# Optimization experiments

Measured on AMD Instinct MI355X. Metric: run time of the kernel, lower is better.

Reference implementation:

```python
import jax, jax.numpy as jnp
import numpy as np
from jax import lax

B, T, D_MODEL = 4, 2048, 2048
EXPAND, D_CONV = 2, 4
D_INNER = D_MODEL * EXPAND


def setup_inputs() -> dict:
    key = jax.random.key(0)
    ks = jax.random.split(key, 5)
    x = jax.random.normal(ks[0], (B, T, D_MODEL), dtype=jnp.float32)
    w_in = jax.random.normal(ks[1], (2 * D_INNER, D_MODEL), dtype=jnp.float32) * (D_MODEL ** -0.5)
    w_out = jax.random.normal(ks[2], (D_MODEL, D_INNER), dtype=jnp.float32) * (D_INNER ** -0.5)
    conv_w = jax.random.normal(ks[3], (D_INNER, 1, D_CONV), dtype=jnp.float32) * (D_CONV ** -0.5)
    conv_b = jax.random.normal(ks[4], (D_INNER,), dtype=jnp.float32) * 0.02
    D = jnp.ones((D_INNER,), dtype=jnp.float32)
    return {"x": x, "w_in": w_in, "w_out": w_out, "conv_w": conv_w, "conv_b": conv_b, "D": D}


def _forward(x, w_in, w_out, conv_w, conv_b, D):
    # in_proj: [B,T,C] @ [C, 2*d_inner]
    x_proj = jnp.einsum('btc,dc->btd', x, w_in)
    xi, gate = jnp.split(x_proj, 2, axis=-1)  # each [B,T,d_inner]
    # depthwise causal conv1d: torch pads both sides by d_conv-1 then truncates
    # output to first T positions -> equivalent to left-pad (d_conv-1), valid conv.
    xc = jnp.transpose(xi, (0, 2, 1))  # [B, d_inner, T]
    xc = lax.conv_general_dilated(
        xc, conv_w,
        window_strides=(1,),
        padding=[(D_CONV - 1, 0)],
        dimension_numbers=('NCH', 'OIH', 'NCH'),
        feature_group_count=D_INNER,
    ) + conv_b[None, :, None]
    xc = jnp.transpose(xc, (0, 2, 1))  # [B, T, d_inner]
    h = jax.nn.silu(xc) * D[None, None, :] * jax.nn.silu(gate)
    return jnp.einsum('btd,cd->btc', h, w_out)


def reference(x, w_in, w_out, conv_w, conv_b, D):
    return _forward(x, w_in, w_out, conv_w, conv_b, D)
```

## Files before the change

### kernel.cpp

```cpp
#include <hip/hip_runtime.h>
#include <hip/hip_bf16.h>
#include <stdint.h>
#include <string.h>


#define BT_TOTAL 8192
#define DM 2048
#define DI 4096

typedef __attribute__((ext_vector_type(8)))  short short8;
typedef __attribute__((ext_vector_type(16))) float f32x16;

__device__ __forceinline__ void async_ld16(const void* g, void* l) {
    __builtin_amdgcn_global_load_lds(
        (__attribute__((address_space(1))) void*)g,
        (__attribute__((address_space(3))) void*)l,
        16, 0, 0);
}

__device__ __forceinline__ float bf2f(ushort u) {
    union { uint i; float f; } v; v.i = ((uint)u) << 16; return v.f;
}

__device__ __forceinline__ ushort f2bf_bits(float f) {
    union { __hip_bfloat16 b; ushort u; } v;
    v.b = __float2bfloat16(f);
    return v.u;
}

#define RA0 0
#define RB0 16384
#define RA1 32768
#define RB1 49152

#define BAR()   asm volatile("s_barrier" ::: "memory")
#define VM6()   asm volatile("s_waitcnt vmcnt(6)" ::: "memory")
#define VM0()   asm volatile("s_waitcnt vmcnt(0)" ::: "memory")
#define PRIO1() __builtin_amdgcn_s_setprio(1)
#define PRIO0() __builtin_amdgcn_s_setprio(0)

template<bool OUT_BF16>
__global__ __launch_bounds__(512, 2) void gemm256_kernel(
    const ushort* __restrict__ A, const ushort* __restrict__ B,
    void* __restrict__ Cp, int M, int N, int K)
{
    __shared__ ushort lds[65536];

    const int tid  = threadIdx.x;
    const int lane = tid & 63;
    const int wave = tid >> 6;
    const int wm   = wave >> 2;
    const int wn   = wave & 3;
    const int l31  = lane & 31;
    const int half = lane >> 5;

    const int nbx = gridDim.x;
    const int nwg = nbx * gridDim.y;
    const int orig = blockIdx.y * nbx + blockIdx.x;
    const int xcd  = orig & 7;
    const int t    = orig >> 3;
    const int sloc = t >> 5;
    const int u    = t & 31;
    const int spx  = (nwg >> 5) >> 3;
    const int g    = xcd * spx + sloc;
    const int scols = nbx >> 2;
    const int sr   = g / scols;
    const int sc   = g - sr * scols;
    const int bm   = (sr * 8 + (u >> 2)) * 256;
    const int bn   = (sc * 4 + (u & 3)) * 256;

    const int rq = tid >> 3;
    const int jq = tid & 7;
    const int fq = (rq ^ (rq >> 3)) & 7;
    const int goffA = (bm + rq) * K + ((jq ^ fq) * 8);
    const int goffB = (bn + rq) * K + ((jq ^ fq) * 8);
    const int dst8  = tid * 8;

    const int flane = (l31 ^ (l31 >> 3)) & 7;
    const int cl8   = (half ^ flane) * 8;
    const int aBase = (wm * 128 + l31) * 64;
    const int bBase = (wn * 64  + l31) * 64;

    f32x16 acc[4][2];
#pragma unroll
    for (int m = 0; m < 4; ++m)
#pragma unroll
        for (int n = 0; n < 2; ++n)
#pragma unroll
            for (int r = 0; r < 16; ++r)
                acc[m][n][r] = 0.f;

    short8 aE[4], aO[4], b0[4], b1[4];

#define STA(P, QROW, REG) async_ld16((P) + (size_t)(QROW) * K + goffA, \
                                     &lds[(REG) + (QROW) * 64 + dst8])
#define STB(P, QROW, REG) async_ld16((P) + (size_t)(QROW) * K + goffB, \
                                     &lds[(REG) + (QROW) * 64 + dst8])

#define RDA(MH, REG) do { \
    _Pragma("unroll") \
    for (int ks = 0; ks < 4; ++ks) { \
        aE[ks] = *(const short8*)&lds[(REG) + aBase + (MH)*4096 + (cl8 ^ (ks<<4))]; \
        aO[ks] = *(const short8*)&lds[(REG) + aBase + (MH)*4096 + 2048 + (cl8 ^ (ks<<4) ^ 32)]; \
    } } while (0)

#define RDB(DSTV, NF, REG) do { \
    _Pragma("unroll") \
    for (int ks = 0; ks < 4; ++ks) { \
        DSTV[ks] = *(const short8*)&lds[(REG) + bBase + (NF)*2048 + (cl8 ^ (ks<<4) ^ ((NF)<<5))]; \
    } } while (0)

#define MMA(MH, NH, BF) do { \
    _Pragma("unroll") \
    for (int ks = 0; ks < 4; ++ks) { \
        acc[(MH)*2    ][(NH)] = __builtin_amdgcn_mfma_f32_32x32x16_bf16( \
            aE[ks], BF[ks], acc[(MH)*2    ][(NH)], 0, 0, 0); \
        acc[(MH)*2 + 1][(NH)] = __builtin_amdgcn_mfma_f32_32x32x16_bf16( \
            aO[ks], BF[ks], acc[(MH)*2 + 1][(NH)], 0, 0, 0); \
    } } while (0)

    {
        STA(A, 0, RA0);  STA(A, 128, RA0);
        STB(B, 0, RB0);  STB(B, 128, RB0);
        STA(A, 64, RA0); STA(A, 192, RA0);
        STB(B, 64, RB0); STB(B, 192, RB0);
        const ushort* Ap = A + 64;
        const ushort* Bp = B + 64;
        STA(Ap, 0, RA1);  STA(Ap, 128, RA1);
        STB(Bp, 0, RB1);  STB(Bp, 128, RB1);
        STA(Ap, 64, RA1); STA(Ap, 192, RA1);
        VM6(); BAR();
    }

    const int NITER = K >> 7;
    for (int i = 0; i < NITER; ++i) {
        const bool last = (i == NITER - 1);
        const int k1 = 128 * i + 64;
        const int k2 = 128 * i + 128;
        const int k3 = 128 * i + 192;

        RDA(0, RA0); RDB(b0, 0, RB0);
        STB(B + k1, 64, RB1); STB(B + k1, 192, RB1);
        PRIO1(); MMA(0, 0, b0); PRIO0();
        BAR();

        RDB(b1, 1, RB0);
        if (!last) { STA(A + k2, 0, RA0); STA(A + k2, 128, RA0); }
        PRIO1(); MMA(0, 1, b1); PRIO0();
        BAR();

        RDA(1, RA0);
        if (!last) { STB(B + k2, 0, RB0); STB(B + k2, 128, RB0); }
        PRIO1(); MMA(1, 1, b1); PRIO0();
        BAR();

        if (!last) { STA(A + k2, 64, RA0); STA(A + k2, 192, RA0); }
        PRIO1(); MMA(1, 0, b0); PRIO0();
        if (last) { VM0(); } else { VM6(); }
        BAR();

        RDA(0, RA1); RDB(b0, 0, RB1);
        if (!last) { STB(B + k2, 64, RB0); STB(B + k2, 192, RB0); }
        PRIO1(); MMA(0, 0, b0); PRIO0();
        BAR();

        RDB(b1, 1, RB1);
        if (!last) { STA(A + k3, 0, RA1); STA(A + k3, 128, RA1); }
        PRIO1(); MMA(0, 1, b1); PRIO0();
        BAR();

        RDA(1, RA1);
        if (!last) { STB(B + k3, 0, RB1); STB(B + k3, 128, RB1); }
        PRIO1(); MMA(1, 1, b1); PRIO0();
        BAR();

        if (!last) { STA(A + k3, 64, RA1); STA(A + k3, 192, RA1); }
        PRIO1(); MMA(1, 0, b0); PRIO0();
        if (!last) { VM6(); BAR(); }
    }

    const int col0 = bn + wn * 64 + l31;
    const int row0 = bm + wm * 128 + 4 * half;
    if (OUT_BF16) {
        __hip_bfloat16* C = (__hip_bfloat16*)Cp;
#pragma unroll
        for (int m = 0; m < 4; ++m)
#pragma unroll
            for (int n = 0; n < 2; ++n)
#pragma unroll
                for (int r = 0; r < 16; ++r) {
                    const int row = row0 + m * 32 + (r & 3) + 8 * (r >> 2);
                    C[(size_t)row * (size_t)N + col0 + n * 32] =
                        __float2bfloat16(acc[m][n][r]);
                }
    } else {
        float* C = (float*)Cp;
#pragma unroll
        for (int m = 0; m < 4; ++m)
#pragma unroll
            for (int n = 0; n < 2; ++n)
#pragma unroll
                for (int r = 0; r < 16; ++r) {
                    const int row = row0 + m * 32 + (r & 3) + 8 * (r >> 2);
                    C[(size_t)row * (size_t)N + col0 + n * 32] = acc[m][n][r];
                }
    }
}

__global__ __launch_bounds__(256) void conv_silu_kernel(
    const ushort* __restrict__ xp,
    const float* __restrict__ cw,
    const float* __restrict__ cb,
    const float* __restrict__ Dv,
    ushort* __restrict__ h)
{
    const int v  = blockIdx.x * 256 + threadIdx.x;
    const int d8 = (v & 511) * 8;
    const int bt = v >> 9;
    const int t  = bt & 2047;

    const uint4 gv = *(const uint4*)(xp + (size_t)bt * (2 * DI) + DI + d8);
    uint4 tap[4];
#pragma unroll
    for (int k = 0; k < 4; ++k) {
        const int tt = t - 3 + k;
        if (tt >= 0)
            tap[k] = *(const uint4*)(xp + (size_t)(bt - 3 + k) * (2 * DI) + d8);
        else
            tap[k] = (uint4){0u, 0u, 0u, 0u};
    }

    const float4* cwv = (const float4*)(cw + (size_t)d8 * 4);
    const float4  cb0 = *(const float4*)(cb + d8);
    const float4  cb1 = *(const float4*)(cb + d8 + 4);
    const float4  dv0 = *(const float4*)(Dv + d8);
    const float4  dv1 = *(const float4*)(Dv + d8 + 4);
    const float cbs[8] = {cb0.x, cb0.y, cb0.z, cb0.w, cb1.x, cb1.y, cb1.z, cb1.w};
    const float dvs[8] = {dv0.x, dv0.y, dv0.z, dv0.w, dv1.x, dv1.y, dv1.z, dv1.w};

    ushort res[8];
#pragma unroll
    for (int j = 0; j < 8; ++j) {
        float a = cbs[j];
        const float4 w = cwv[j];
        const float wk[4] = {w.x, w.y, w.z, w.w};
#pragma unroll
        for (int k = 0; k < 4; ++k) {
            const uint u = ((const uint*)&tap[k])[j >> 1];
            const ushort us = (j & 1) ? (ushort)(u >> 16) : (ushort)(u & 0xffff);
            a += bf2f(us) * wk[k];
        }
        const uint gu = ((const uint*)&gv)[j >> 1];
        const ushort gs = (j & 1) ? (ushort)(gu >> 16) : (ushort)(gu & 0xffff);
        const float g = bf2f(gs);
        const float sc = a / (1.f + __expf(-a));
        const float sg = g / (1.f + __expf(-g));
        res[j] = f2bf_bits(sc * dvs[j] * sg);
    }
    *(uint4*)(h + (size_t)bt * DI + d8) = *(const uint4*)res;
}

__global__ __launch_bounds__(256) void f32_to_bf16_x4(
    const float* __restrict__ in, __hip_bfloat16* __restrict__ out, int n4)
{
    const int i = blockIdx.x * 256 + threadIdx.x;
    if (i >= n4) return;
    const float4 v = *(const float4*)(in + (size_t)i * 4);
    union { __hip_bfloat16 hh[4]; ushort4 u; } cv;
    cv.hh[0] = __float2bfloat16(v.x);
    cv.hh[1] = __float2bfloat16(v.y);
    cv.hh[2] = __float2bfloat16(v.z);
    cv.hh[3] = __float2bfloat16(v.w);
    *(ushort4*)((ushort*)out + (size_t)i * 4) = cv.u;
}

extern "C" void kernel_launch(void* const* d_in, const int* in_sizes, int n_in,
                              void* d_out, int out_size, void* d_ws, size_t ws_size,
                              hipStream_t stream)
{
    const float* x     = (const float*)d_in[0];
    const float* w_in  = (const float*)d_in[1];
    const float* w_out = (const float*)d_in[2];
    const float* cw    = (const float*)d_in[3];
    const float* cb    = (const float*)d_in[4];
    const float* Dv    = (const float*)d_in[5];
    float* out = (float*)d_out;

    char* wsc = (char*)d_ws;
    __hip_bfloat16* xproj = (__hip_bfloat16*)wsc;
    __hip_bfloat16* xb    = (__hip_bfloat16*)(wsc + (size_t)134217728);
    __hip_bfloat16* winb  = (__hip_bfloat16*)(wsc + (size_t)134217728 + 33554432);
    __hip_bfloat16* hbuf  = (__hip_bfloat16*)(wsc + (size_t)134217728);
    __hip_bfloat16* woutb = (__hip_bfloat16*)(wsc + (size_t)201326592);

    f32_to_bf16_x4<<<(BT_TOTAL * DM / 4 + 255) / 256, 256, 0, stream>>>(x, xb, BT_TOTAL * DM / 4);
    f32_to_bf16_x4<<<(2 * DI * DM / 4 + 255) / 256, 256, 0, stream>>>(w_in, winb, 2 * DI * DM / 4);
    f32_to_bf16_x4<<<(DM * DI / 4 + 255) / 256, 256, 0, stream>>>(w_out, woutb, DM * DI / 4);

    gemm256_kernel<true><<<dim3((2 * DI) / 256, BT_TOTAL / 256), 512, 0, stream>>>(
        (const ushort*)xb, (const ushort*)winb, xproj, BT_TOTAL, 2 * DI, DM);

    conv_silu_kernel<<<(BT_TOTAL * DI / 8) / 256, 256, 0, stream>>>(
        (const ushort*)xproj, cw, cb, Dv, (ushort*)hbuf);

    gemm256_kernel<false><<<dim3(DM / 256, BT_TOTAL / 256), 512, 0, stream>>>(
        (const ushort*)hbuf, (const ushort*)woutb, out, BT_TOTAL, DM, DI);
}
```

Baseline: 613.4 us.

## Restructure GEMM main loop into four coarser phases with fewer barriers

```diff
diff --git a/kernel.cpp b/kernel.cpp
--- a/kernel.cpp
+++ b/kernel.cpp
@@ -34,7 +34,7 @@
 #define RB1 49152
 
 #define BAR()   asm volatile("s_barrier" ::: "memory")
-#define VM6()   asm volatile("s_waitcnt vmcnt(6)" ::: "memory")
+#define VM4()   asm volatile("s_waitcnt vmcnt(4)" ::: "memory")
 #define VM0()   asm volatile("s_waitcnt vmcnt(0)" ::: "memory")
 #define PRIO1() __builtin_amdgcn_s_setprio(1)
 #define PRIO0() __builtin_amdgcn_s_setprio(0)
@@ -128,55 +128,42 @@
         const ushort* Bp = B + 64;
         STA(Ap, 0, RA1);  STA(Ap, 128, RA1);
         STB(Bp, 0, RB1);  STB(Bp, 128, RB1);
-        STA(Ap, 64, RA1); STA(Ap, 192, RA1);
-        VM6(); BAR();
+        VM4(); BAR();
     }
 
     const int NITER = K >> 7;
     for (int i = 0; i < NITER; ++i) {
         const bool last = (i == NITER - 1);
-        const int k1 = 128 * i + 64;
-        const int k2 = 128 * i + 128;
-        const int k3 = 128 * i + 192;
+        const int kT1 = 128 * i + 64;
+        const int kT2 = 128 * i + 128;
+        const int kT3 = 128 * i + 192;
 
         RDA(0, RA0); RDB(b0, 0, RB0);
-        STB(B + k1, 64, RB1); STB(B + k1, 192, RB1);
-        PRIO1(); MMA(0, 0, b0); PRIO0();
+        STB(B + kT1, 64, RB1); STB(B + kT1, 192, RB1);
+        STA(A + kT1, 64, RA1); STA(A + kT1, 192, RA1);
+        RDB(b1, 1, RB0);
+        PRIO1(); MMA(0, 0, b0); MMA(0, 1, b1); PRIO0();
+        RDA(1, RA0);
         BAR();
 
-        RDB(b1, 1, RB0);
-        if (!last) { STA(A + k2, 0, RA0); STA(A + k2, 128, RA0); }
-        PRIO1(); MMA(0, 1, b1); PRIO0();
+        if (!last) { STA(A + kT2, 0, RA0); STA(A + kT2, 128, RA0);
+                     STB(B + kT2, 0, RB0); STB(B + kT2, 128, RB0); }
+        PRIO1(); MMA(1, 1, b1); MMA(1, 0, b0); PRIO0();
+        if (last) { VM0(); } else { VM4(); }
         BAR();
 
-        RDA(1, RA0);
-        if (!last) { STB(B + k2, 0, RB0); STB(B + k2, 128, RB0); }
-        PRIO1(); MMA(1, 1, b1); PRIO0();
+        RDA(0, RA1); RDB(b0, 0, RB1);
+        if (!last) { STB(B + kT2, 64, RB0); STB(B + kT2, 192, RB0);
+                     STA(A + kT2, 64, RA0); STA(A + kT2, 192, RA0); }
+        RDB(b1, 1, RB1);
+        PRIO1(); MMA(0, 0, b0); MMA(0, 1, b1); PRIO0();
+        RDA(1, RA1);
         BAR();
 
-        if (!last) { STA(A + k2, 64, RA0); STA(A + k2, 192, RA0); }
-        PRIO1(); MMA(1, 0, b0); PRIO0();
-        if (last) { VM0(); } else { VM6(); }
-        BAR();
-
-        RDA(0, RA1); RDB(b0, 0, RB1);
-        if (!last) { STB(B + k2, 64, RB0); STB(B + k2, 192, RB0); }
-        PRIO1(); MMA(0, 0, b0); PRIO0();
-        BAR();
-
-        RDB(b1, 1, RB1);
-        if (!last) { STA(A + k3, 0, RA1); STA(A + k3, 128, RA1); }
-        PRIO1(); MMA(0, 1, b1); PRIO0();
-        BAR();
-
-        RDA(1, RA1);
-        if (!last) { STB(B + k3, 0, RB1); STB(B + k3, 128, RB1); }
-        PRIO1(); MMA(1, 1, b1); PRIO0();
-        BAR();
-
-        if (!last) { STA(A + k3, 64, RA1); STA(A + k3, 192, RA1); }
-        PRIO1(); MMA(1, 0, b0); PRIO0();
-        if (!last) { VM6(); BAR(); }
+        if (!last) { STA(A + kT3, 0, RA1); STA(A + kT3, 128, RA1);
+                     STB(B + kT3, 0, RB1); STB(B + kT3, 128, RB1); }
+        PRIO1(); MMA(1, 1, b1); MMA(1, 0, b0); PRIO0();
+        if (!last) { VM4(); BAR(); }
     }
 
     const int col0 = bn + wn * 64 + l31;
```

Result: slower. 650.4 us (+6.0%).
